# Kernel tuning notes

Measured on AMD Instinct MI355X. Metric: run time of the kernel, lower is better.

Reference implementation:

```python
import jax, jax.numpy as jnp
import numpy as np

BATCH = 16384
NUM_INPUTS = 128
# features = squares (n) + singles (n) + pairs C(n,2)
NUM_FEATS = NUM_INPUTS + NUM_INPUTS + (NUM_INPUTS * (NUM_INPUTS - 1)) // 2  # 8384

# precompute pair index lists (equivalent to itertools.combinations(range(n), 2))
_II, _JJ = np.triu_indices(NUM_INPUTS, k=1)
_II = jnp.asarray(_II)
_JJ = jnp.asarray(_JJ)


def setup_inputs() -> dict:
    key = jax.random.key(0)
    k1, k2 = jax.random.split(key)
    x = jax.random.normal(k1, (BATCH, NUM_INPUTS), dtype=jnp.float32)
    w = jax.random.normal(k2, (NUM_FEATS,), dtype=jnp.float32) * 0.05
    return {"x": x, "w": w}


def reference(x, w):
    # order=2, with_squares=True
    # squares block: o=1 -> inputs**2 / 1**2
    sq = x * x
    # combination order 1: f = 1! -> x / 1
    singles = x
    # combination order 2: f = 2! -> x_i * x_j / 2 for all i<j (combinations order)
    pairs = (x[:, _II] * x[:, _JJ]) * jnp.float32(0.5)
    t = jnp.concatenate([sq, singles, pairs], axis=-1)  # [B, 8384]
    return t * w
```

## Files before the change

kernel.cpp:

```cpp
#include <hip/hip_runtime.h>


constexpr int BATCH = 16384;
constexpr int NIN   = 128;
constexpr int NFEAT = NIN + NIN + (NIN * (NIN - 1)) / 2;
constexpr int BROWS = 32;
constexpr int TPB   = 256;

__device__ __forceinline__ int pair_off(int i) {
    return i * (NIN - 1) - (i * (i - 1)) / 2;
}

__global__ __launch_bounds__(TPB) void cpl_kernel(const float* __restrict__ x,
                                                  const float* __restrict__ w,
                                                  float* __restrict__ out) {
    __shared__ float xs[BROWS * NIN];

    const int tid = threadIdx.x;
    const int b0  = blockIdx.y * BROWS;

    {
        const float4* src = reinterpret_cast<const float4*>(x + (size_t)b0 * NIN);
        float4*       dst = reinterpret_cast<float4*>(xs);
#pragma unroll
        for (int k = 0; k < (BROWS * NIN / 4) / TPB; ++k)
            dst[k * TPB + tid] = src[k * TPB + tid];
    }
    __syncthreads();

    const int f = blockIdx.x * TPB + tid;
    if (f >= NFEAT) return;

    int i1, i2, mode;
    if (f < NIN) {
        i1 = f; i2 = f; mode = 0;
    } else if (f < 2 * NIN) {
        i1 = f - NIN; i2 = f - NIN; mode = 1;
    } else {
        const int p = f - 2 * NIN;
        float s = sqrtf((float)(65025 - 8 * p));
        int   i = (int)((255.0f - s) * 0.5f);
        i = min(max(i, 0), NIN - 2);
        while (pair_off(i + 1) <= p) ++i;
        while (pair_off(i) > p)      --i;
        i1 = i;
        i2 = i + 1 + (p - pair_off(i));
        mode = 2;
    }
    const float wf = w[f];

    float* op = out + (size_t)b0 * NFEAT + f;
#pragma unroll
    for (int b = 0; b < BROWS; ++b) {
        const float xi = xs[b * NIN + i1];
        const float xj = xs[b * NIN + i2];
        float p = xi * xj;
        if (mode == 1) p = xi;
        if (mode == 2) p *= 0.5f;
        op[(size_t)b * NFEAT] = p * wf;
    }
}

extern "C" void kernel_launch(void* const* d_in, const int* in_sizes, int n_in,
                              void* d_out, int out_size, void* d_ws, size_t ws_size,
                              hipStream_t stream) {
    const float* x = (const float*)d_in[0];
    const float* w = (const float*)d_in[1];
    float*     out = (float*)d_out;

    dim3 block(TPB);
    dim3 grid((NFEAT + TPB - 1) / TPB,
              BATCH / BROWS);
    cpl_kernel<<<grid, block, 0, stream>>>(x, w, out);
}
```

Measured before the change: 101.7 us.

## Precompute pair index table and restructure grid to row-blocks looping over features

Adds a setup kernel that decodes each feature into a packed (i,j) index pair and a pre-scaled weight, storing both in workspace. The main kernel now has one block per 8 rows that loops over all features, prefetching the next table entry. Singles are handled by multiplying with a constant 1.0 column in shared memory, which removes branches. This cuts the per-feature sqrt-based index decode and gives each block a larger contiguous write region, at the cost of an extra launch and a smaller per-block row tile.

New measurement: 115.5 us. +13.5%, slower.

```diff
diff --git a/kernel.cpp b/kernel.cpp
--- a/kernel.cpp
+++ b/kernel.cpp
@@ -1,63 +1,85 @@
 #include <hip/hip_runtime.h>
 
 
-constexpr int BATCH = 16384;
-constexpr int NIN   = 128;
-constexpr int NFEAT = NIN + NIN + (NIN * (NIN - 1)) / 2;
-constexpr int BROWS = 32;
-constexpr int TPB   = 256;
+constexpr int BATCH   = 16384;
+constexpr int NIN     = 128;
+constexpr int NFEAT   = NIN + NIN + (NIN * (NIN - 1)) / 2;
+constexpr int TPB     = 256;
+constexpr int ROWS    = 8;
+constexpr int RSTRIDE = 132;
+constexpr int KITERS  = (NFEAT + TPB - 1) / TPB;
 
 __device__ __forceinline__ int pair_off(int i) {
     return i * (NIN - 1) - (i * (i - 1)) / 2;
 }
 
+__device__ __forceinline__ void decode_f(int f, float w, int& i, int& j, float& ws) {
+    if (f < NIN)          { i = f;       j = f;   ws = w; }
+    else if (f < 2 * NIN) { i = f - NIN; j = NIN; ws = w; }
+    else {
+        const int p = f - 2 * NIN;
+        float s = sqrtf((float)(65025 - 8 * p));
+        int  ii = (int)((255.0f - s) * 0.5f);
+        ii = min(max(ii, 0), NIN - 2);
+        while (pair_off(ii + 1) <= p) ++ii;
+        while (pair_off(ii)     >  p) --ii;
+        i = ii; j = ii + 1 + (p - pair_off(ii));
+        ws = w * 0.5f;
+    }
+}
+
+__global__ void setup_kernel(const float* __restrict__ w,
+                             float* __restrict__ wsb,
+                             unsigned short* __restrict__ tbl) {
+    const int f = blockIdx.x * TPB + threadIdx.x;
+    if (f >= NFEAT) return;
+    int i, j; float ws;
+    decode_f(f, w[f], i, j, ws);
+    wsb[f] = ws;
+    tbl[f] = (unsigned short)((i << 8) | j);
+}
+
+template <bool USE_TBL>
 __global__ __launch_bounds__(TPB) void cpl_kernel(const float* __restrict__ x,
                                                   const float* __restrict__ w,
+                                                  const float* __restrict__ wsb,
+                                                  const unsigned short* __restrict__ tbl,
                                                   float* __restrict__ out) {
-    __shared__ float xs[BROWS * NIN];
-
+    __shared__ float xs[ROWS * RSTRIDE];
     const int tid = threadIdx.x;
-    const int b0  = blockIdx.y * BROWS;
+    const int r0  = blockIdx.x * ROWS;
 
     {
-        const float4* src = reinterpret_cast<const float4*>(x + (size_t)b0 * NIN);
-        float4*       dst = reinterpret_cast<float4*>(xs);
-#pragma unroll
-        for (int k = 0; k < (BROWS * NIN / 4) / TPB; ++k)
-            dst[k * TPB + tid] = src[k * TPB + tid];
+        const int r = tid >> 5, c = (tid & 31) * 4;
+        float4 v = *reinterpret_cast<const float4*>(x + (size_t)(r0 + r) * NIN + c);
+        *reinterpret_cast<float4*>(&xs[r * RSTRIDE + c]) = v;
     }
+    if (tid < ROWS) xs[tid * RSTRIDE + NIN] = 1.0f;
     __syncthreads();
 
-    const int f = blockIdx.x * TPB + tid;
-    if (f >= NFEAT) return;
+    unsigned short e_nx = 0; float w_nx = 0.0f;
+    if (USE_TBL) { e_nx = tbl[tid]; w_nx = wsb[tid]; }
 
-    int i1, i2, mode;
-    if (f < NIN) {
-        i1 = f; i2 = f; mode = 0;
-    } else if (f < 2 * NIN) {
-        i1 = f - NIN; i2 = f - NIN; mode = 1;
-    } else {
-        const int p = f - 2 * NIN;
-        float s = sqrtf((float)(65025 - 8 * p));
-        int   i = (int)((255.0f - s) * 0.5f);
-        i = min(max(i, 0), NIN - 2);
-        while (pair_off(i + 1) <= p) ++i;
-        while (pair_off(i) > p)      --i;
-        i1 = i;
-        i2 = i + 1 + (p - pair_off(i));
-        mode = 2;
-    }
-    const float wf = w[f];
-
-    float* op = out + (size_t)b0 * NFEAT + f;
+    for (int k = 0; k < KITERS; ++k) {
+        const int f = k * TPB + tid;
+        int i, j; float ws;
+        if (USE_TBL) {
+            const unsigned short e = e_nx; ws = w_nx;
+            const int fn = min(f + TPB, NFEAT - 1);
+            e_nx = tbl[fn]; w_nx = wsb[fn];
+            i = e >> 8; j = e & 255;
+        } else {
+            if (f < NFEAT) decode_f(f, w[f], i, j, ws);
+            else           { i = 0; j = 0; ws = 0.0f; }
+        }
+        if (f < NFEAT) {
+            float* op = out + (size_t)r0 * NFEAT + f;
 #pragma unroll
-    for (int b = 0; b < BROWS; ++b) {
-        const float xi = xs[b * NIN + i1];
-        const float xj = xs[b * NIN + i2];
-        float p = xi * xj;
-        if (mode == 1) p = xi;
-        if (mode == 2) p *= 0.5f;
-        op[(size_t)b * NFEAT] = p * wf;
+            for (int r = 0; r < ROWS; ++r) {
+                const float* xr = &xs[r * RSTRIDE];
+                op[(size_t)r * NFEAT] = xr[i] * xr[j] * ws;
+            }
+        }
     }
 }
 
@@ -68,8 +90,16 @@
     const float* w = (const float*)d_in[1];
     float*     out = (float*)d_out;
 
-    dim3 block(TPB);
-    dim3 grid((NFEAT + TPB - 1) / TPB,
-              BATCH / BROWS);
-    cpl_kernel<<<grid, block, 0, stream>>>(x, w, out);
+    const size_t need = (size_t)NFEAT * sizeof(float) + (size_t)NFEAT * sizeof(unsigned short);
+    float*          wsb = (float*)d_ws;
+    unsigned short* tbl = (unsigned short*)((char*)d_ws + (size_t)NFEAT * sizeof(float));
+
+    const dim3 grid(BATCH / ROWS);
+
+    if (ws_size >= need) {
+        setup_kernel<<<(NFEAT + TPB - 1) / TPB, TPB, 0, stream>>>(w, wsb, tbl);
+        cpl_kernel<true><<<grid, TPB, 0, stream>>>(x, w, wsb, tbl, out);
+    } else {
+        cpl_kernel<false><<<grid, TPB, 0, stream>>>(x, w, wsb, tbl, out);
+    }
 }
```

## Vectorize output stores to float4 per thread with swizzled shared layout

Applied to the files above, without the earlier changes.

Each thread now computes four consecutive features and writes them with a single 128-bit store per batch row, instead of scalar stores. The x tile in shared memory is stored in a swizzled, padded layout with a constant-1 column, so singles, squares and pairs all use one multiply path without mode branches. The aim is fewer store instructions and less index overhead. In exchange there are fewer threads per launch and more registers per thread.

Result: slower. 110.6 us (+8.7%).

```diff
diff --git a/kernel.cpp b/kernel.cpp
--- a/kernel.cpp
+++ b/kernel.cpp
@@ -3,61 +3,77 @@
 
 constexpr int BATCH = 16384;
 constexpr int NIN   = 128;
-constexpr int NFEAT = NIN + NIN + (NIN * (NIN - 1)) / 2;
+constexpr int NPAIR = NIN * (NIN - 1) / 2;
+constexpr int NFEAT = 2 * NIN + NPAIR;
+constexpr int NQUAD = NFEAT / 4;
+constexpr int TPB   = 256;
 constexpr int BROWS = 32;
-constexpr int TPB   = 256;
+constexpr int RS    = 132;
 
-__device__ __forceinline__ int pair_off(int i) {
-    return i * (NIN - 1) - (i * (i - 1)) / 2;
-}
+__device__ __forceinline__ int swz(int c) { return (c & 3) * 32 + (c >> 2); }
+__device__ __forceinline__ int pair_off(int i) { return i * (NIN - 1) - (i * (i - 1)) / 2; }
 
 __global__ __launch_bounds__(TPB) void cpl_kernel(const float* __restrict__ x,
                                                   const float* __restrict__ w,
                                                   float* __restrict__ out) {
-    __shared__ float xs[BROWS * NIN];
+    __shared__ float xs[BROWS * RS];
+    const int tid = threadIdx.x;
+    const int r0  = blockIdx.y * BROWS;
 
-    const int tid = threadIdx.x;
-    const int b0  = blockIdx.y * BROWS;
-
-    {
-        const float4* src = reinterpret_cast<const float4*>(x + (size_t)b0 * NIN);
-        float4*       dst = reinterpret_cast<float4*>(xs);
 #pragma unroll
-        for (int k = 0; k < (BROWS * NIN / 4) / TPB; ++k)
-            dst[k * TPB + tid] = src[k * TPB + tid];
+    for (int p = 0; p < BROWS * 32 / TPB; ++p) {
+        const int r  = p * (TPB / 32) + (tid >> 5);
+        const int c4 = (tid & 31) * 4;
+        float4 v = *reinterpret_cast<const float4*>(x + (size_t)(r0 + r) * NIN + c4);
+        float* row = &xs[r * RS];
+        row[0 * 32 + (tid & 31)] = v.x;
+        row[1 * 32 + (tid & 31)] = v.y;
+        row[2 * 32 + (tid & 31)] = v.z;
+        row[3 * 32 + (tid & 31)] = v.w;
     }
+    if (tid < BROWS) xs[tid * RS + 128] = 1.0f;
     __syncthreads();
 
-    const int f = blockIdx.x * TPB + tid;
-    if (f >= NFEAT) return;
+    const int qd = blockIdx.x * TPB + tid;
+    if (qd >= NQUAD) return;
+    const int f0 = qd * 4;
 
-    int i1, i2, mode;
-    if (f < NIN) {
-        i1 = f; i2 = f; mode = 0;
-    } else if (f < 2 * NIN) {
-        i1 = f - NIN; i2 = f - NIN; mode = 1;
+    const float4 w4 = *reinterpret_cast<const float4*>(w + f0);
+    const float* wp = reinterpret_cast<const float*>(&w4);
+    int   ia[4], ib[4];
+    float ws[4];
+    if (f0 < NIN) {
+#pragma unroll
+        for (int q = 0; q < 4; ++q) { ia[q] = swz(f0 + q); ib[q] = ia[q]; ws[q] = wp[q]; }
+    } else if (f0 < 2 * NIN) {
+#pragma unroll
+        for (int q = 0; q < 4; ++q) { ia[q] = swz(f0 - NIN + q); ib[q] = 128; ws[q] = wp[q]; }
     } else {
-        const int p = f - 2 * NIN;
-        float s = sqrtf((float)(65025 - 8 * p));
+        const int p0 = f0 - 2 * NIN;
+        float s = sqrtf((float)(65025 - 8 * p0));
         int   i = (int)((255.0f - s) * 0.5f);
         i = min(max(i, 0), NIN - 2);
-        while (pair_off(i + 1) <= p) ++i;
-        while (pair_off(i) > p)      --i;
-        i1 = i;
-        i2 = i + 1 + (p - pair_off(i));
-        mode = 2;
+        while (pair_off(i + 1) <= p0) ++i;
+        while (pair_off(i)     >  p0) --i;
+        int j = i + 1 + (p0 - pair_off(i));
+#pragma unroll
+        for (int q = 0; q < 4; ++q) {
+            ia[q] = swz(i); ib[q] = swz(j); ws[q] = wp[q] * 0.5f;
+            if (++j > NIN - 1) { ++i; j = i + 1; }
+        }
     }
-    const float wf = w[f];
 
-    float* op = out + (size_t)b0 * NFEAT + f;
-#pragma unroll
-    for (int b = 0; b < BROWS; ++b) {
-        const float xi = xs[b * NIN + i1];
-        const float xj = xs[b * NIN + i2];
-        float p = xi * xj;
-        if (mode == 1) p = xi;
-        if (mode == 2) p *= 0.5f;
-        op[(size_t)b * NFEAT] = p * wf;
+    float* op = out + (size_t)r0 * NFEAT + f0;
+#pragma unroll 4
+    for (int r = 0; r < BROWS; ++r) {
+        const float* xr = &xs[r * RS];
+        float4 v;
+        v.x = xr[ia[0]] * xr[ib[0]] * ws[0];
+        v.y = xr[ia[1]] * xr[ib[1]] * ws[1];
+        v.z = xr[ia[2]] * xr[ib[2]] * ws[2];
+        v.w = xr[ia[3]] * xr[ib[3]] * ws[3];
+        *reinterpret_cast<float4*>(op) = v;
+        op += NFEAT;
     }
 }
 
@@ -68,8 +84,7 @@
     const float* w = (const float*)d_in[1];
     float*     out = (float*)d_out;
 
-    dim3 block(TPB);
-    dim3 grid((NFEAT + TPB - 1) / TPB,
+    dim3 grid((NQUAD + TPB - 1) / TPB,
               BATCH / BROWS);
-    cpl_kernel<<<grid, block, 0, stream>>>(x, w, out);
+    cpl_kernel<<<grid, TPB, 0, stream>>>(x, w, out);
 }
```

## Drop shared-memory staging, read x directly from global, double rows per block

Applied to the files above, without the earlier changes.

Removes the LDS tile and barrier, so each thread reads its two x values straight from global memory (served from L1/L2) for every row. Rows per block go from 32 to 64, and the pair scale of 0.5 is folded into the weight. This cuts the per-block cooperative load and sync, at the cost of gathered global loads. It also halves the grid's row dimension, which reduces parallelism.

Result: slower. 167.3 us (+64.5%).

```diff
diff --git a/kernel.cpp b/kernel.cpp
--- a/kernel.cpp
+++ b/kernel.cpp
@@ -3,61 +3,47 @@
 
 constexpr int BATCH = 16384;
 constexpr int NIN   = 128;
-constexpr int NFEAT = NIN + NIN + (NIN * (NIN - 1)) / 2;
-constexpr int BROWS = 32;
+constexpr int NFEAT = 2 * NIN + NIN * (NIN - 1) / 2;
 constexpr int TPB   = 256;
+constexpr int BROWS = 64;
 
-__device__ __forceinline__ int pair_off(int i) {
-    return i * (NIN - 1) - (i * (i - 1)) / 2;
-}
+__device__ __forceinline__ int pair_off(int i) { return i * (NIN - 1) - (i * (i - 1)) / 2; }
 
 __global__ __launch_bounds__(TPB) void cpl_kernel(const float* __restrict__ x,
                                                   const float* __restrict__ w,
                                                   float* __restrict__ out) {
-    __shared__ float xs[BROWS * NIN];
+    const int tid = threadIdx.x;
+    const int f   = blockIdx.x * TPB + tid;
+    if (f >= NFEAT) return;
+    const int r0 = blockIdx.y * BROWS;
 
-    const int tid = threadIdx.x;
-    const int b0  = blockIdx.y * BROWS;
-
-    {
-        const float4* src = reinterpret_cast<const float4*>(x + (size_t)b0 * NIN);
-        float4*       dst = reinterpret_cast<float4*>(xs);
-#pragma unroll
-        for (int k = 0; k < (BROWS * NIN / 4) / TPB; ++k)
-            dst[k * TPB + tid] = src[k * TPB + tid];
-    }
-    __syncthreads();
-
-    const int f = blockIdx.x * TPB + tid;
-    if (f >= NFEAT) return;
-
-    int i1, i2, mode;
+    int  i1, i2;
+    bool single = false;
+    float ws;
     if (f < NIN) {
-        i1 = f; i2 = f; mode = 0;
+        i1 = f; i2 = f; ws = w[f];
     } else if (f < 2 * NIN) {
-        i1 = f - NIN; i2 = f - NIN; mode = 1;
+        i1 = f - NIN; i2 = i1; ws = w[f]; single = true;
     } else {
         const int p = f - 2 * NIN;
         float s = sqrtf((float)(65025 - 8 * p));
         int   i = (int)((255.0f - s) * 0.5f);
         i = min(max(i, 0), NIN - 2);
         while (pair_off(i + 1) <= p) ++i;
-        while (pair_off(i) > p)      --i;
+        while (pair_off(i)     >  p) --i;
         i1 = i;
         i2 = i + 1 + (p - pair_off(i));
-        mode = 2;
+        ws = w[f] * 0.5f;
     }
-    const float wf = w[f];
 
-    float* op = out + (size_t)b0 * NFEAT + f;
+    const float* xp = x + (size_t)r0 * NIN;
+    float*       op = out + (size_t)r0 * NFEAT + f;
 #pragma unroll
-    for (int b = 0; b < BROWS; ++b) {
-        const float xi = xs[b * NIN + i1];
-        const float xj = xs[b * NIN + i2];
-        float p = xi * xj;
-        if (mode == 1) p = xi;
-        if (mode == 2) p *= 0.5f;
-        op[(size_t)b * NFEAT] = p * wf;
+    for (int r = 0; r < BROWS; ++r) {
+        float xi = xp[(size_t)r * NIN + i1];
+        float xj = xp[(size_t)r * NIN + i2];
+        if (single) xj = 1.0f;
+        op[(size_t)r * NFEAT] = xi * xj * ws;
     }
 }
 
@@ -68,8 +54,7 @@
     const float* w = (const float*)d_in[1];
     float*     out = (float*)d_out;
 
-    dim3 block(TPB);
     dim3 grid((NFEAT + TPB - 1) / TPB,
               BATCH / BROWS);
-    cpl_kernel<<<grid, block, 0, stream>>>(x, w, out);
+    cpl_kernel<<<grid, TPB, 0, stream>>>(x, w, out);
 }
```
